# Kernel optimization log

Hardware: AMD Instinct MI355X
Metric: run time of the kernel (lower is better)

## Reference

```python
import jax, jax.numpy as jnp
import numpy as np

N = 6000      # nodes
E = 150000    # edges (avg degree ~25, close to _AVG_DEGREE=23.4)
K = 9         # (lmax+1)^2 spherical coefficients, lmax=2
C = 128       # sphere_channels
H = 8         # num_heads
V = 16        # attn_value_channels (H*V == C)
L = 2         # num_layers
B = 512       # num_distance_basis
RMAX = 5.0
EPS = 1e-6


def _rms_sh(x):
    # rms_norm_sh-style normalization over (coefficients, channels)
    return x * jax.lax.rsqrt(jnp.mean(x * x, axis=(-2, -1), keepdims=True) + EPS)


def _seg_softmax(logits, seg, n):
    # numerically-stable per-destination-node softmax over incoming edges
    m = jax.ops.segment_max(logits, seg, num_segments=n)
    ex = jnp.exp(logits - m[seg])
    s = jax.ops.segment_sum(ex, seg, num_segments=n)
    return ex / (s[seg] + 1e-9)


def setup_inputs() -> dict:
    key = jax.random.key(0)
    ks = jax.random.split(key, 24)
    s = 0.02
    inp = {
        # graph / features
        "atom_feats": jax.random.randint(ks[0], (N, 4), 0, 10),
        "bond_feats": jax.random.randint(ks[1], (E, 3), 0, 8),
        "edge_index": jax.random.randint(ks[2], (2, E), 0, N),
        "edge_distance": jax.random.uniform(ks[3], (E,), jnp.float32, 0.0, RMAX),
        # embeddings
        "atom_emb": jax.random.normal(ks[4], (4, 10, C), jnp.float32) * s,
        "bond_emb": jax.random.normal(ks[5], (3, 8, C), jnp.float32) * s,
        # distance-basis edge MLP (edge_channels_list = [512, 128, 128])
        "W_rbf1": jax.random.normal(ks[6], (B, C), jnp.float32) * s,
        "b_rbf1": jnp.zeros((C,), jnp.float32),
        "W_rbf2": jax.random.normal(ks[7], (C, C), jnp.float32) * s,
        "b_rbf2": jnp.zeros((C,), jnp.float32),
        # per-layer attention params (stacked over L)
        "Wa1": jax.random.normal(ks[8], (L, 3 * C, C), jnp.float32) * s,
        "Wa2": jax.random.normal(ks[9], (L, C, H), jnp.float32) * s,
        "Wv": jax.random.normal(ks[10], (L, C, H * V), jnp.float32) * s,
        "Wg": jax.random.normal(ks[11], (L, C, H), jnp.float32) * s,
        "Wo": jax.random.normal(ks[12], (L, H * V, C), jnp.float32) * s,
        # per-layer FFN params
        "Wf1": jax.random.normal(ks[13], (L, C, 512), jnp.float32) * s,
        "Wf2": jax.random.normal(ks[14], (L, 512, C), jnp.float32) * s,
    }
    return inp


def _forward(atom_feats, bond_feats, edge_index, edge_distance,
             atom_emb, bond_emb, W_rbf1, b_rbf1, W_rbf2, b_rbf2,
             Wa1, Wa2, Wv, Wg, Wo, Wf1, Wf2):
    src, dst = edge_index[0], edge_index[1]

    # --- atom embedding into l=0 coefficient of the SH node state ---
    a0 = sum(atom_emb[f][atom_feats[:, f]] for f in range(4))      # [N, C]
    x = jnp.zeros((N, K, C), a0.dtype).at[:, 0, :].set(a0)          # [N, K, C]

    # --- gaussian distance basis + edge embedding MLP + bond features ---
    centers = jnp.linspace(0.0, RMAX, B)
    width = RMAX / B
    rbf = jnp.exp(-((edge_distance[:, None] - centers[None, :]) / width) ** 2)  # [E, B]
    e = jax.nn.silu(rbf @ W_rbf1 + b_rbf1) @ W_rbf2 + b_rbf2                    # [E, C]
    e = e + sum(bond_emb[f][bond_feats[:, f]] for f in range(3))

    for l in range(L):
        # ---- SO(2)-style graph attention block ----
        xn = _rms_sh(x)
        xs = xn[src]                                                 # [E, K, C] gather
        inv = jnp.concatenate([xn[src, 0], xn[dst, 0], e], axis=-1)  # invariant feats [E, 3C]
        logits = jax.nn.silu(inv @ Wa1[l]) @ Wa2[l]                  # [E, H]
        alpha = _seg_softmax(logits, dst, N)                         # renormalized attention
        gate = jax.nn.sigmoid(e @ Wg[l])                             # edge-embedding gate [E, H]
        v = jnp.einsum('ekc,chv->ekhv', xs, Wv[l].reshape(C, H, V))  # [E, K, H, V]
        v = v * (alpha * gate)[:, None, :, None]
        msg = v.reshape(E, K, H * V)
        agg = jax.ops.segment_sum(msg, dst, num_segments=N)          # scatter [N, K, H*V]
        x = x + jnp.einsum('nkd,dc->nkc', agg, Wo[l])

        # ---- equivariant FFN with separable S2-style activation ----
        xn = _rms_sh(x)
        h = jnp.einsum('nkc,cf->nkf', xn, Wf1[l])                    # [N, K, 512]
        h0 = jax.nn.silu(h[:, :1, :])                                # l=0 scalar path
        hr = h[:, 1:, :] * jax.nn.sigmoid(h[:, :1, :])               # gated l>0 path
        h = jnp.concatenate([h0, hr], axis=1)
        x = x + jnp.einsum('nkf,fc->nkc', h, Wf2[l])

    return _rms_sh(x)


def reference(atom_feats, bond_feats, edge_index, edge_distance,
              atom_emb, bond_emb, W_rbf1, b_rbf1, W_rbf2, b_rbf2,
              Wa1, Wa2, Wv, Wg, Wo, Wf1, Wf2):
    return _forward(atom_feats, bond_feats, edge_index, edge_distance,
                    atom_emb, bond_emb, W_rbf1, b_rbf1, W_rbf2, b_rbf2,
                    Wa1, Wa2, Wv, Wg, Wo, Wf1, Wf2)
```

## Files before the change

kernel.cpp:

```cpp
#include <hip/hip_runtime.h>

#define NN 6000
#define NE 150000
#define TBM 2048
#define TROWS (TBM + 1)

typedef unsigned int uint;
typedef unsigned short ushort;
typedef __attribute__((ext_vector_type(8))) short short8v;
typedef __attribute__((ext_vector_type(4))) float float4v;

__device__ __forceinline__ float siluf(float x) { return x / (1.f + __expf(-x)); }
__device__ __forceinline__ float sigmf(float x) { return 1.f / (1.f + __expf(-x)); }
__device__ __forceinline__ uint pack2bf(float lo, float hi) {
    uint ul = __float_as_uint(lo);
    ul = (ul + 0x7fffu + ((ul >> 16) & 1u)) >> 16;
    uint uh = __float_as_uint(hi);
    uh = ((uh + 0x7fffu + ((uh >> 16) & 1u)) >> 16) << 16;
    return ul | uh;
}
__device__ __forceinline__ ushort f2bf(float f) {
    uint u = __float_as_uint(f);
    return (ushort)((u + 0x7fffu + ((u >> 16) & 1u)) >> 16);
}
__device__ __forceinline__ float2 up2(uint u) {
    return make_float2(__uint_as_float(u << 16), __uint_as_float(u & 0xffff0000u));
}

__global__ __launch_bounds__(256)
void k_prep(const float* __restrict__ W2, const float* __restrict__ b2,
            const float* __restrict__ Wa1, const float* __restrict__ Wg,
            const float* __restrict__ bemb,
            const float* __restrict__ Wf1, const float* __restrict__ Wf2,
            const float* __restrict__ Wv, const float* __restrict__ Wa2,
            const float* __restrict__ Wo,
            float* __restrict__ W2A, float* __restrict__ W2G,
            float* __restrict__ bA, float* __restrict__ bG,
            uint* __restrict__ BAcb, float* __restrict__ BGc,
            ushort* __restrict__ Wf1x, ushort* __restrict__ Wf2x,
            ushort* __restrict__ Wvx, ushort* __restrict__ Wa1sx,
            ushort* __restrict__ Wa1dx, ushort* __restrict__ Wa2x,
            ushort* __restrict__ Wox, int* __restrict__ deg)
{
    __shared__ float w2_s[8][132];
    const int l = blockIdx.y, bx = blockIdx.x, tid = threadIdx.x;
    const float* Wa1e = Wa1 + (size_t)l * 384 * 128 + 256 * 128;
    const float* Wgl  = Wg  + (size_t)l * 128 * 8;

    if (bx < 16) {
        const int i0 = bx * 8;
        for (int q = tid; q < 8 * 32; q += 256) {
            int ni = q >> 5, j4 = (q & 31) * 4;
            *reinterpret_cast<float4*>(&w2_s[ni][j4]) =
                *reinterpret_cast<const float4*>(&W2[(size_t)(i0 + ni) * 128 + j4]);
        }
        __syncthreads();
        const int j = tid & 127, ng = tid >> 7;
        float a[4] = {0.f, 0.f, 0.f, 0.f};
        #pragma unroll 4
        for (int k4 = 0; k4 < 128; k4 += 4) {
            float w0 = Wa1e[(k4 + 0) * 128 + j];
            float w1 = Wa1e[(k4 + 1) * 128 + j];
            float w2v = Wa1e[(k4 + 2) * 128 + j];
            float w3 = Wa1e[(k4 + 3) * 128 + j];
            #pragma unroll
            for (int r = 0; r < 4; ++r) {
                const float4 xv = *reinterpret_cast<const float4*>(&w2_s[ng * 4 + r][k4]);
                a[r] += xv.x * w0 + xv.y * w1 + xv.z * w2v + xv.w * w3;
            }
        }
        #pragma unroll
        for (int r = 0; r < 4; ++r)
            W2A[(size_t)l * 16384 + (size_t)(i0 + ng * 4 + r) * 128 + j] = a[r];
    } else if (bx == 16) {
        const int i = tid & 127, hq = tid >> 7;
        float a[4] = {0.f, 0.f, 0.f, 0.f};
        for (int k = 0; k < 128; ++k) {
            float w = W2[(size_t)i * 128 + k];
            const float4 g4 = *reinterpret_cast<const float4*>(&Wgl[k * 8 + hq * 4]);
            a[0] += w * g4.x; a[1] += w * g4.y; a[2] += w * g4.z; a[3] += w * g4.w;
        }
        #pragma unroll
        for (int q = 0; q < 4; ++q)
            W2G[(size_t)l * 1024 + (size_t)i * 8 + hq * 4 + q] = a[q];
    } else if (bx == 17) {
        if (tid < 128) {
            float s = 0.f;
            for (int k = 0; k < 128; ++k) s += b2[k] * Wa1e[k * 128 + tid];
            bA[l * 128 + tid] = s;
        } else if (tid < 136) {
            int h = tid - 128;
            float s = 0.f;
            for (int k = 0; k < 128; ++k) s += b2[k] * Wgl[k * 8 + h];
            bG[l * 8 + h] = s;
        } else if (l == 0) {
            for (int i = tid - 136; i < NN; i += 120) if (i >= 0) deg[i] = 0;
        }
    } else if (bx < 274) {
        const int cb = (bx - 18) * 2 + (tid >> 7);
        const int c = tid & 127;
        const int b[3] = {cb >> 6, (cb >> 3) & 7, cb & 7};
        float s = 0.f;
        #pragma unroll
        for (int f = 0; f < 3; ++f) {
            const float* er = &bemb[(size_t)(f * 8 + b[f]) * 128];
            for (int k = 0; k < 128; ++k)
                s += er[k] * Wa1e[k * 128 + c];
        }
        float hi = __shfl_down(s, 1, 64);
        if ((c & 1) == 0)
            BAcb[(size_t)l * 512 * 64 + (size_t)cb * 64 + (c >> 1)] = pack2bf(s, hi);
        if (c < 8) {
            float g = 0.f;
            #pragma unroll
            for (int f = 0; f < 3; ++f) {
                const float* er = &bemb[(size_t)(f * 8 + b[f]) * 128];
                for (int k = 0; k < 128; ++k)
                    g += er[k] * Wgl[k * 8 + c];
            }
            BGc[(size_t)l * 512 * 8 + (size_t)cb * 8 + c] = g;
        }
    } else {
        const int sub = (bx - 274) * 4 + (tid >> 6);
        const int lane = tid & 63;
        if (sub < 128) {
            const int nt = sub >> 2, kt = sub & 3;
            const float* src = Wf1 + (size_t)l * 65536;
            ushort* dst = Wf1x + (size_t)l * 65536 + ((size_t)sub * 64 + lane) * 8;
            #pragma unroll
            for (int j = 0; j < 8; ++j)
                dst[j] = f2bf(src[(size_t)(kt * 32 + (lane >> 4) * 8 + j) * 512 + nt * 16 + (lane & 15)]);
        } else if (sub < 256) {
            const int b2x = sub - 128;
            const int nt = b2x >> 4, kt = b2x & 15;
            const float* src = Wf2 + (size_t)l * 65536;
            ushort* dst = Wf2x + (size_t)l * 65536 + ((size_t)b2x * 64 + lane) * 8;
            #pragma unroll
            for (int j = 0; j < 8; ++j)
                dst[j] = f2bf(src[(size_t)(kt * 32 + (lane >> 4) * 8 + j) * 128 + nt * 16 + (lane & 15)]);
        } else if (sub < 352) {
            const int b3 = sub - 256;
            const int mat = b3 >> 5, blk = b3 & 31;
            const int nt = blk >> 2, kt = blk & 3;
            const float* src;
            ushort* dst;
            if (mat == 0)      { src = Wv  + (size_t)l * 16384;             dst = Wvx   + (size_t)l * 16384; }
            else if (mat == 1) { src = Wa1 + (size_t)l * 384 * 128;         dst = Wa1sx + (size_t)l * 16384; }
            else               { src = Wa1 + (size_t)l * 384 * 128 + 16384; dst = Wa1dx + (size_t)l * 16384; }
            dst += ((size_t)blk * 64 + lane) * 8;
            #pragma unroll
            for (int j = 0; j < 8; ++j)
                dst[j] = f2bf(src[(size_t)(kt * 32 + (lane >> 4) * 8 + j) * 128 + nt * 16 + (lane & 15)]);
        } else if (sub < 356) {
            const int kt = sub - 352;
            const int col = lane & 15;
            const float* src = Wa2 + (size_t)l * 128 * 8;
            ushort* dst = Wa2x + (size_t)l * 2048 + ((size_t)kt * 64 + lane) * 8;
            #pragma unroll
            for (int j = 0; j < 8; ++j) {
                int krow = kt * 32 + (lane >> 4) * 8 + j;
                dst[j] = (col < 8) ? f2bf(src[(size_t)krow * 8 + col]) : (ushort)0;
            }
        } else {
            const int blk = sub - 356;
            const int nt = blk >> 2, kt = blk & 3;
            const float* src = Wo + (size_t)l * 16384;
            ushort* dst = Wox + (size_t)l * 16384 + ((size_t)blk * 64 + lane) * 8;
            #pragma unroll
            for (int j = 0; j < 8; ++j)
                dst[j] = f2bf(src[(size_t)(kt * 32 + (lane >> 4) * 8 + j) * 128 + nt * 16 + (lane & 15)]);
        }
    }
}

__device__ __forceinline__
void node_gemm3(const ushort a_s[16][136], int tid, int n0,
                const ushort* __restrict__ Wvx, const ushort* __restrict__ Wa1sx,
                const ushort* __restrict__ Wa1dx,
                uint* __restrict__ Vb, uint* __restrict__ Psb, uint* __restrict__ Pdb)
{
    const int l = tid & 63, wq = tid >> 6;
    const int lr = l & 15, lk = l >> 4;
    #pragma unroll
    for (int jb = 0; jb < 6; ++jb) {
        int job = wq * 6 + jb;
        int mat = job >> 3, nt = job & 7;
        const ushort* W = (mat == 0) ? Wvx : (mat == 1 ? Wa1sx : Wa1dx);
        uint* O = (mat == 0) ? Vb : (mat == 1 ? Psb : Pdb);
        float4v acc = (float4v){0.f, 0.f, 0.f, 0.f};
        #pragma unroll
        for (int ks = 0; ks < 4; ++ks) {
            short8v af = *reinterpret_cast<const short8v*>(&a_s[lr][lk * 8 + ks * 32]);
            short8v bf = *reinterpret_cast<const short8v*>(&W[((size_t)(nt * 4 + ks) * 64 + l) * 8]);
            acc = __builtin_amdgcn_mfma_f32_16x16x32_bf16(af, bf, acc, 0, 0, 0);
        }
        #pragma unroll
        for (int r = 0; r < 4; ++r) {
            float v = acc[r];
            float vn = __shfl_xor(v, 1, 64);
            if ((l & 1) == 0) {
                int row = lk * 4 + r, col = nt * 16 + lr;
                O[(size_t)(n0 + row) * 64 + (col >> 1)] = pack2bf(v, vn);
            }
        }
    }
}

__device__ __forceinline__
void node_gemm3_8w(const ushort a_s[16][136], int tid, int n0,
                   const ushort* __restrict__ Wvx, const ushort* __restrict__ Wa1sx,
                   const ushort* __restrict__ Wa1dx,
                   uint* __restrict__ Vb, uint* __restrict__ Psb, uint* __restrict__ Pdb)
{
    const int l = tid & 63, w = tid >> 6;
    const int lr = l & 15, lk = l >> 4;
    #pragma unroll
    for (int jb = 0; jb < 3; ++jb) {
        int job = w * 3 + jb;
        int mat = job >> 3, nt = job & 7;
        const ushort* W = (mat == 0) ? Wvx : (mat == 1 ? Wa1sx : Wa1dx);
        uint* O = (mat == 0) ? Vb : (mat == 1 ? Psb : Pdb);
        float4v acc = (float4v){0.f, 0.f, 0.f, 0.f};
        #pragma unroll
        for (int ks = 0; ks < 4; ++ks) {
            short8v af = *reinterpret_cast<const short8v*>(&a_s[lr][lk * 8 + ks * 32]);
            short8v bf = *reinterpret_cast<const short8v*>(&W[((size_t)(nt * 4 + ks) * 64 + l) * 8]);
            acc = __builtin_amdgcn_mfma_f32_16x16x32_bf16(af, bf, acc, 0, 0, 0);
        }
        #pragma unroll
        for (int r = 0; r < 4; ++r) {
            float v = acc[r];
            float vn = __shfl_xor(v, 1, 64);
            if ((l & 1) == 0) {
                int row = lk * 4 + r, col = nt * 16 + lr;
                O[(size_t)(n0 + row) * 64 + (col >> 1)] = pack2bf(v, vn);
            }
        }
    }
}

__global__ __launch_bounds__(256)
void k_prep2(const float* __restrict__ W1, const float* __restrict__ b1,
             const float* __restrict__ W2A, const float* __restrict__ W2G,
             const float* __restrict__ bA, const float* __restrict__ bG,
             uint* __restrict__ TAb, float* __restrict__ TG,
             const int* __restrict__ af, const float* __restrict__ aemb,
             float* __restrict__ x, int* __restrict__ deg,
             const int* __restrict__ eidx,
             const ushort* __restrict__ Wvx, const ushort* __restrict__ Wa1sx,
             const ushort* __restrict__ Wa1dx,
             uint* __restrict__ Vb, uint* __restrict__ Psb, uint* __restrict__ Pdb)
{
    __shared__ float rbf_s[8][32];
    __shared__ int   bs_s[8];
    __shared__ float t1_s[8][132];
    __shared__ ushort a_s[16][136];
    const int tid = threadIdx.x, bx = blockIdx.x;

    if (bx < 514) {
        const int l = (bx >= 257) ? 1 : 0;
        const int r0 = (bx - l * 257) * 8;
        {
            int ri = tid >> 5, j = tid & 31;
            int row = min(r0 + ri, TBM);
            float d = (float)row * (5.0f / TBM);
            const float step = 5.0f / 511.0f;
            const float invw = 512.0f / 5.0f;
            int b0 = (int)(d * (511.0f / 5.0f) + 0.5f);
            int bs = min(max(b0 - 16, 0), 512 - 32);
            if (j == 0) bs_s[ri] = bs;
            float z = (d - (float)(bs + j) * step) * invw;
            rbf_s[ri][j] = __expf(-z * z);
        }
        __syncthreads();
        #pragma unroll
        for (int pass = 0; pass < 4; ++pass) {
            int idx = pass * 256 + tid;
            int ri = idx >> 7, c = idx & 127;
            int bs = bs_s[ri];
            float t = b1[c];
            #pragma unroll
            for (int j = 0; j < 32; ++j)
                t += rbf_s[ri][j] * W1[(bs + j) * 128 + c];
            t1_s[ri][c] = siluf(t);
        }
        __syncthreads();

        const float* W2Al = W2A + (size_t)l * 16384;
        const int c = tid & 127, ng = tid >> 7;
        float a[4];
        #pragma unroll
        for (int r = 0; r < 4; ++r) a[r] = bA[l * 128 + c];
        #pragma unroll 4
        for (int k4 = 0; k4 < 128; k4 += 4) {
            float w0 = W2Al[(k4 + 0) * 128 + c];
            float w1 = W2Al[(k4 + 1) * 128 + c];
            float w2v = W2Al[(k4 + 2) * 128 + c];
            float w3 = W2Al[(k4 + 3) * 128 + c];
            #pragma unroll
            for (int r = 0; r < 4; ++r) {
                const float4 xv = *reinterpret_cast<const float4*>(&t1_s[ng * 4 + r][k4]);
                a[r] += xv.x * w0 + xv.y * w1 + xv.z * w2v + xv.w * w3;
            }
        }
        #pragma unroll
        for (int r = 0; r < 4; ++r) {
            float hi = __shfl_down(a[r], 1, 64);
            int row = r0 + ng * 4 + r;
            if (((c & 1) == 0) && row <= TBM)
                TAb[(size_t)l * TROWS * 64 + (size_t)row * 64 + (c >> 1)] = pack2bf(a[r], hi);
        }
        if (tid < 64) {
            int ri = tid >> 3, h = tid & 7;
            int row = r0 + ri;
            if (row <= TBM) {
                const float* W2Gl = W2G + (size_t)l * 1024;
                float s = bG[l * 8 + h];
                #pragma unroll 8
                for (int k = 0; k < 128; ++k)
                    s += t1_s[ri][k] * W2Gl[k * 8 + h];
                TG[(size_t)l * TROWS * 8 + (size_t)row * 8 + h] = s;
            }
        }
    } else if (bx < 889) {
        const int n0 = (bx - 514) * 16;
        {
            int ni = tid >> 4, c8 = (tid & 15) * 8;
            int n = n0 + ni;
            float v[8];
            #pragma unroll
            for (int q = 0; q < 8; ++q) v[q] = 0.f;
            #pragma unroll
            for (int f = 0; f < 4; ++f) {
                int idx = af[n * 4 + f];
                const float* er = &aemb[(size_t)(f * 10 + idx) * 128 + c8];
                float4 e0 = *reinterpret_cast<const float4*>(er);
                float4 e1 = *reinterpret_cast<const float4*>(er + 4);
                v[0] += e0.x; v[1] += e0.y; v[2] += e0.z; v[3] += e0.w;
                v[4] += e1.x; v[5] += e1.y; v[6] += e1.z; v[7] += e1.w;
            }
            float* xr = &x[(size_t)n * 128 + c8];
            *reinterpret_cast<float4*>(xr)     = make_float4(v[0], v[1], v[2], v[3]);
            *reinterpret_cast<float4*>(xr + 4) = make_float4(v[4], v[5], v[6], v[7]);
            float ss = 0.f;
            #pragma unroll
            for (int q = 0; q < 8; ++q) ss += v[q] * v[q];
            #pragma unroll
            for (int m = 1; m < 16; m <<= 1) ss += __shfl_xor(ss, m, 16);
            float r = rsqrtf(ss * (1.0f / 1152.0f) + 1e-6f);
            uint4 pk;
            pk.x = pack2bf(v[0] * r, v[1] * r);
            pk.y = pack2bf(v[2] * r, v[3] * r);
            pk.z = pack2bf(v[4] * r, v[5] * r);
            pk.w = pack2bf(v[6] * r, v[7] * r);
            *reinterpret_cast<uint4*>(&a_s[ni][c8]) = pk;
        }
        __syncthreads();
        node_gemm3(a_s, tid, n0, Wvx, Wa1sx, Wa1dx, Vb, Psb, Pdb);
    } else {
        int e = (bx - 889) * 256 + tid;
        if (e < NE) atomicAdd(&deg[eidx[NE + e]], 1);
    }
}

__global__ __launch_bounds__(1024)
void k_scan(const int* __restrict__ deg, int* __restrict__ off, int* __restrict__ cursor)
{
    __shared__ int part[1024];
    const int t = threadIdx.x;
    const int base = t * 6;
    int loc[6]; int s = 0;
    #pragma unroll
    for (int i = 0; i < 6; ++i) {
        int d = (base + i < NN) ? deg[base + i] : 0;
        loc[i] = s; s += d;
    }
    part[t] = s;
    __syncthreads();
    for (int o = 1; o < 1024; o <<= 1) {
        int v = (t >= o) ? part[t - o] : 0;
        __syncthreads();
        part[t] += v;
        __syncthreads();
    }
    int pre = (t > 0) ? part[t - 1] : 0;
    #pragma unroll
    for (int i = 0; i < 6; ++i) {
        if (base + i < NN) {
            int v = pre + loc[i];
            off[base + i] = v;
            cursor[base + i] = v;
        }
    }
    if (t == 1023) off[NN] = part[1023];
}

__global__ __launch_bounds__(256)
void k_fill(const int* __restrict__ eidx, const int* __restrict__ bondf,
            const float* __restrict__ dist, int* __restrict__ cursor,
            int* __restrict__ srcp, int4* __restrict__ erec)
{
    int e = blockIdx.x * 256 + threadIdx.x;
    if (e < NE) {
        int d = eidx[NE + e];
        int p = atomicAdd(&cursor[d], 1);
        int sn = eidx[e];
        srcp[p] = sn;
        erec[p] = make_int4(sn, d, __float_as_int(dist[e]),
                            bondf[e * 3 + 0] * 64 + bondf[e * 3 + 1] * 8 + bondf[e * 3 + 2]);
    }
}

__global__ __launch_bounds__(256)
void k_attn(const int4* __restrict__ erec,
            const uint* __restrict__ Psb, const uint* __restrict__ Pdb,
            const uint* __restrict__ TAbl, const float* __restrict__ TGl,
            const uint* __restrict__ BAcbl, const float* __restrict__ BGcl,
            const ushort* __restrict__ Wa2xl,
            uint* __restrict__ nexp)
{
    __shared__ ushort t_s[64][136];
    __shared__ float gate_s[64][8];
    const int tid = threadIdx.x;
    const int p0 = blockIdx.x * 64;

    #pragma unroll
    for (int half = 0; half < 2; ++half) {
        const int ei = (tid >> 3) + half * 32;
        const int g = tid & 7;
        const int p = min(p0 + ei, NE - 1);
        const int4 er = erec[p];
        const int sn = er.x, dn = er.y;
        const float d = __int_as_float(er.z);
        const int cb = er.w;
        float u = d * ((float)TBM / 5.0f);
        int i = min((int)u, TBM - 1);
        float f = u - (float)i, f1 = 1.f - f;

        uint ps[8], pd[8], t0[8], t1v[8], ba[8];
        {
            const uint4* pp = reinterpret_cast<const uint4*>(&Psb[(size_t)sn * 64 + g * 8]);
            uint4 a = pp[0], b = pp[1];
            ps[0]=a.x; ps[1]=a.y; ps[2]=a.z; ps[3]=a.w; ps[4]=b.x; ps[5]=b.y; ps[6]=b.z; ps[7]=b.w;
            pp = reinterpret_cast<const uint4*>(&Pdb[(size_t)dn * 64 + g * 8]);
            a = pp[0]; b = pp[1];
            pd[0]=a.x; pd[1]=a.y; pd[2]=a.z; pd[3]=a.w; pd[4]=b.x; pd[5]=b.y; pd[6]=b.z; pd[7]=b.w;
            pp = reinterpret_cast<const uint4*>(&TAbl[(size_t)i * 64 + g * 8]);
            a = pp[0]; b = pp[1];
            t0[0]=a.x; t0[1]=a.y; t0[2]=a.z; t0[3]=a.w; t0[4]=b.x; t0[5]=b.y; t0[6]=b.z; t0[7]=b.w;
            pp = reinterpret_cast<const uint4*>(&TAbl[(size_t)(i + 1) * 64 + g * 8]);
            a = pp[0]; b = pp[1];
            t1v[0]=a.x; t1v[1]=a.y; t1v[2]=a.z; t1v[3]=a.w; t1v[4]=b.x; t1v[5]=b.y; t1v[6]=b.z; t1v[7]=b.w;
            pp = reinterpret_cast<const uint4*>(&BAcbl[(size_t)cb * 64 + g * 8]);
            a = pp[0]; b = pp[1];
            ba[0]=a.x; ba[1]=a.y; ba[2]=a.z; ba[3]=a.w; ba[4]=b.x; ba[5]=b.y; ba[6]=b.z; ba[7]=b.w;
        }
        uint tw[8];
        #pragma unroll
        for (int q = 0; q < 8; ++q) {
            float2 vs = up2(ps[q]), vd = up2(pd[q]), v0 = up2(t0[q]), v1 = up2(t1v[q]), vb = up2(ba[q]);
            float s0 = siluf(vs.x + vd.x + f1 * v0.x + f * v1.x + vb.x);
            float s1 = siluf(vs.y + vd.y + f1 * v0.y + f * v1.y + vb.y);
            tw[q] = pack2bf(s0, s1);
        }
        uint4* tp = reinterpret_cast<uint4*>(&t_s[ei][g * 16]);
        tp[0] = make_uint4(tw[0], tw[1], tw[2], tw[3]);
        tp[1] = make_uint4(tw[4], tw[5], tw[6], tw[7]);
        if (g == 0) {
            const float4* tg0 = reinterpret_cast<const float4*>(&TGl[(size_t)i * 8]);
            const float4* bg4 = reinterpret_cast<const float4*>(&BGcl[(size_t)cb * 8]);
            #pragma unroll
            for (int q = 0; q < 2; ++q) {
                float4 g0 = tg0[q], g1 = tg0[q + 2], bb = bg4[q];
                gate_s[ei][4 * q + 0] = f1 * g0.x + f * g1.x + bb.x;
                gate_s[ei][4 * q + 1] = f1 * g0.y + f * g1.y + bb.y;
                gate_s[ei][4 * q + 2] = f1 * g0.z + f * g1.z + bb.z;
                gate_s[ei][4 * q + 3] = f1 * g0.w + f * g1.w + bb.w;
            }
        }
    }
    __syncthreads();

    {
        const int wq = tid >> 6, l = tid & 63;
        const int lr = l & 15, lk = l >> 4;
        float4v acc = (float4v){0.f, 0.f, 0.f, 0.f};
        #pragma unroll
        for (int ks = 0; ks < 4; ++ks) {
            short8v af = *reinterpret_cast<const short8v*>(&t_s[wq * 16 + lr][lk * 8 + ks * 32]);
            short8v bf = *reinterpret_cast<const short8v*>(&Wa2xl[((size_t)ks * 64 + l) * 8]);
            acc = __builtin_amdgcn_mfma_f32_16x16x32_bf16(af, bf, acc, 0, 0, 0);
        }
        const int h = l & 15;
        if (h < 8) {
            #pragma unroll
            for (int r = 0; r < 4; ++r) {
                int ei = wq * 16 + lk * 4 + r;
                int p = p0 + ei;
                if (p < NE) {
                    float ex = __expf(acc[r]);
                    nexp[(size_t)p * 8 + h] = pack2bf(ex * sigmf(gate_s[ei][h]), ex);
                }
            }
        }
    }
}

template<int LAST>
__global__ __launch_bounds__(512)
void k_layer_fused(float* __restrict__ x,
                   const int* __restrict__ off, const int* __restrict__ srcp,
                   const uint* __restrict__ nexp, const uint* __restrict__ Vb,
                   const ushort* __restrict__ Woxl,
                   const ushort* __restrict__ Wf1xl, const ushort* __restrict__ Wf2xl,
                   float* __restrict__ out,
                   const ushort* __restrict__ WvxN, const ushort* __restrict__ Wa1sxN,
                   const ushort* __restrict__ Wa1dxN,
                   uint* __restrict__ VbO, uint* __restrict__ Psb, uint* __restrict__ Pdb)
{
    __shared__ ushort a_s[16][136];
    __shared__ ushort h_s[16][520];
    __shared__ float xf_s[16][132];
    const int tid = threadIdx.x;
    const int n0 = blockIdx.x * 16;
    const int ni = tid >> 5;
    const int ci = tid & 31;
    const int c4 = ci * 4;

    {
        *reinterpret_cast<float4*>(&xf_s[ni][c4]) =
            *reinterpret_cast<const float4*>(&x[(size_t)(n0 + ni) * 128 + c4]);
    }

    {
        const int n = n0 + ni;
        const int h = ci >> 2;
        const int cd2 = ci * 2;
        const int s = off[n], t = off[n + 1];
        float a0 = 0.f, a1 = 0.f, a2 = 0.f, a3 = 0.f, es = 0.f;
        int p = s;
        for (; p + 4 <= t; p += 4) {
            int sn0 = srcp[p + 0], sn1 = srcp[p + 1], sn2 = srcp[p + 2], sn3 = srcp[p + 3];
            float2 ne0 = up2(nexp[(size_t)(p + 0) * 8 + h]);
            float2 ne1 = up2(nexp[(size_t)(p + 1) * 8 + h]);
            float2 ne2 = up2(nexp[(size_t)(p + 2) * 8 + h]);
            float2 ne3 = up2(nexp[(size_t)(p + 3) * 8 + h]);
            uint2 u0 = *reinterpret_cast<const uint2*>(&Vb[(size_t)sn0 * 64 + cd2]);
            uint2 u1 = *reinterpret_cast<const uint2*>(&Vb[(size_t)sn1 * 64 + cd2]);
            uint2 u2 = *reinterpret_cast<const uint2*>(&Vb[(size_t)sn2 * 64 + cd2]);
            uint2 u3 = *reinterpret_cast<const uint2*>(&Vb[(size_t)sn3 * 64 + cd2]);
            es += ne0.y + ne1.y + ne2.y + ne3.y;
            float2 v;
            v = up2(u0.x); a0 += ne0.x * v.x; a1 += ne0.x * v.y;
            v = up2(u0.y); a2 += ne0.x * v.x; a3 += ne0.x * v.y;
            v = up2(u1.x); a0 += ne1.x * v.x; a1 += ne1.x * v.y;
            v = up2(u1.y); a2 += ne1.x * v.x; a3 += ne1.x * v.y;
            v = up2(u2.x); a0 += ne2.x * v.x; a1 += ne2.x * v.y;
            v = up2(u2.y); a2 += ne2.x * v.x; a3 += ne2.x * v.y;
            v = up2(u3.x); a0 += ne3.x * v.x; a1 += ne3.x * v.y;
            v = up2(u3.y); a2 += ne3.x * v.x; a3 += ne3.x * v.y;
        }
        for (; p < t; ++p) {
            int sn = srcp[p];
            float2 ne = up2(nexp[(size_t)p * 8 + h]);
            uint2 u = *reinterpret_cast<const uint2*>(&Vb[(size_t)sn * 64 + cd2]);
            es += ne.y;
            float2 v;
            v = up2(u.x); a0 += ne.x * v.x; a1 += ne.x * v.y;
            v = up2(u.y); a2 += ne.x * v.x; a3 += ne.x * v.y;
        }
        float sinv = 1.f / (es + 1e-9f);
        uint2 pk;
        pk.x = pack2bf(a0 * sinv, a1 * sinv);
        pk.y = pack2bf(a2 * sinv, a3 * sinv);
        *reinterpret_cast<uint2*>(&a_s[ni][c4]) = pk;
    }
    __syncthreads();

    const int l  = tid & 63;
    const int w  = tid >> 6;
    const int lr = l & 15, lk = l >> 4;

    {
        float4v acc = (float4v){0.f, 0.f, 0.f, 0.f};
        #pragma unroll
        for (int ks = 0; ks < 4; ++ks) {
            short8v af = *reinterpret_cast<const short8v*>(&a_s[lr][lk * 8 + ks * 32]);
            short8v bf = *reinterpret_cast<const short8v*>(&Woxl[((size_t)(w * 4 + ks) * 64 + l) * 8]);
            acc = __builtin_amdgcn_mfma_f32_16x16x32_bf16(af, bf, acc, 0, 0, 0);
        }
        #pragma unroll
        for (int r = 0; r < 4; ++r)
            xf_s[lk * 4 + r][w * 16 + lr] += acc[r];
    }
    __syncthreads();

    {
        float4 v = *reinterpret_cast<const float4*>(&xf_s[ni][c4]);
        float ss = v.x * v.x + v.y * v.y + v.z * v.z + v.w * v.w;
        #pragma unroll
        for (int m = 1; m < 32; m <<= 1) ss += __shfl_xor(ss, m, 32);
        float r = rsqrtf(ss * (1.0f / 1152.0f) + 1e-6f);
        uint2 pk;
        pk.x = pack2bf(v.x * r, v.y * r);
        pk.y = pack2bf(v.z * r, v.w * r);
        *reinterpret_cast<uint2*>(&a_s[ni][c4]) = pk;
    }
    __syncthreads();

    {
        float4v acc[4];
        #pragma unroll
        for (int nf = 0; nf < 4; ++nf) acc[nf] = (float4v){0.f, 0.f, 0.f, 0.f};
        #pragma unroll
        for (int ks = 0; ks < 4; ++ks) {
            short8v af = *reinterpret_cast<const short8v*>(&a_s[lr][lk * 8 + ks * 32]);
            #pragma unroll
            for (int nf = 0; nf < 4; ++nf) {
                int nt = w * 4 + nf;
                short8v bf = *reinterpret_cast<const short8v*>(&Wf1xl[((size_t)(nt * 4 + ks) * 64 + l) * 8]);
                acc[nf] = __builtin_amdgcn_mfma_f32_16x16x32_bf16(af, bf, acc[nf], 0, 0, 0);
            }
        }
        #pragma unroll
        for (int nf = 0; nf < 4; ++nf) {
            #pragma unroll
            for (int r = 0; r < 4; ++r) {
                float v = siluf(acc[nf][r]);
                float vn = __shfl_xor(v, 1, 64);
                if ((l & 1) == 0) {
                    int row = lk * 4 + r;
                    int col = (w * 4 + nf) * 16 + lr;
                    *reinterpret_cast<uint*>(&h_s[row][col]) = pack2bf(v, vn);
                }
            }
        }
    }
    __syncthreads();

    {
        float4v acc = (float4v){0.f, 0.f, 0.f, 0.f};
        #pragma unroll 4
        for (int ks = 0; ks < 16; ++ks) {
            short8v af = *reinterpret_cast<const short8v*>(&h_s[lr][lk * 8 + ks * 32]);
            short8v bf = *reinterpret_cast<const short8v*>(&Wf2xl[((size_t)(w * 16 + ks) * 64 + l) * 8]);
            acc = __builtin_amdgcn_mfma_f32_16x16x32_bf16(af, bf, acc, 0, 0, 0);
        }
        #pragma unroll
        for (int r = 0; r < 4; ++r)
            xf_s[lk * 4 + r][w * 16 + lr] += acc[r];
    }
    __syncthreads();

    {
        float4 v = *reinterpret_cast<const float4*>(&xf_s[ni][c4]);
        float ss = v.x * v.x + v.y * v.y + v.z * v.z + v.w * v.w;
        #pragma unroll
        for (int m = 1; m < 32; m <<= 1) ss += __shfl_xor(ss, m, 32);
        float r = rsqrtf(ss * (1.0f / 1152.0f) + 1e-6f);

        if (!LAST) {
            *reinterpret_cast<float4*>(&x[(size_t)(n0 + ni) * 128 + c4]) = v;
            uint2 pk;
            pk.x = pack2bf(v.x * r, v.y * r);
            pk.y = pack2bf(v.z * r, v.w * r);
            *reinterpret_cast<uint2*>(&a_s[ni][c4]) = pk;
            __syncthreads();
            node_gemm3_8w(a_s, tid, n0, WvxN, Wa1sxN, Wa1dxN, VbO, Psb, Pdb);
        } else {
            size_t base = (size_t)(n0 + ni) * 1152 + c4;
            *reinterpret_cast<float4*>(&out[base]) = make_float4(v.x * r, v.y * r, v.z * r, v.w * r);
            const float4 z4 = make_float4(0.f, 0.f, 0.f, 0.f);
            #pragma unroll
            for (int k = 1; k < 9; ++k)
                *reinterpret_cast<float4*>(&out[base + (size_t)k * 128]) = z4;
        }
    }
}

extern "C" void kernel_launch(void* const* d_in, const int* in_sizes, int n_in,
                              void* d_out, int out_size, void* d_ws, size_t ws_size,
                              hipStream_t stream)
{
    const int*   atom_feats = (const int*)d_in[0];
    const int*   bond_feats = (const int*)d_in[1];
    const int*   edge_index = (const int*)d_in[2];
    const float* edge_dist  = (const float*)d_in[3];
    const float* atom_emb   = (const float*)d_in[4];
    const float* bond_emb   = (const float*)d_in[5];
    const float* W_rbf1     = (const float*)d_in[6];
    const float* b_rbf1     = (const float*)d_in[7];
    const float* W_rbf2     = (const float*)d_in[8];
    const float* b_rbf2     = (const float*)d_in[9];
    const float* Wa1        = (const float*)d_in[10];
    const float* Wa2        = (const float*)d_in[11];
    const float* Wv         = (const float*)d_in[12];
    const float* Wg         = (const float*)d_in[13];
    const float* Wo         = (const float*)d_in[14];
    const float* Wf1        = (const float*)d_in[15];
    const float* Wf2        = (const float*)d_in[16];
    float* out = (float*)d_out;

    float* ws   = (float*)d_ws;
    float* x    = ws;
    uint* nexp  = (uint*)(x + NN * 128);
    float* W2A  = (float*)(nexp + (size_t)NE * 8);
    float* W2G  = W2A  + 2 * 16384;
    float* bA   = W2G  + 2 * 1024;
    float* bG   = bA   + 2 * 128;
    float* TG   = bG   + 16;
    float* BGc  = TG   + 2 * (size_t)TROWS * 8;
    uint* Vb    = (uint*)(BGc + 2 * 512 * 8);
    uint* Psb   = Vb  + NN * 64;
    uint* Pdb   = Psb + NN * 64;
    uint* TAb   = Pdb + NN * 64;
    uint* BAcb  = TAb + 2 * (size_t)TROWS * 64;
    ushort* Wf1x  = (ushort*)(BAcb + 2 * 512 * 64);
    ushort* Wf2x  = Wf1x  + 2 * 65536;
    ushort* Wvx   = Wf2x  + 2 * 65536;
    ushort* Wa1sx = Wvx   + 2 * 16384;
    ushort* Wa1dx = Wa1sx + 2 * 16384;
    ushort* Wa2x  = Wa1dx + 2 * 16384;
    ushort* Wox   = Wa2x  + 2 * 2048;
    int* deg    = (int*)(Wox + 2 * 16384);
    int* off    = deg + NN;
    int* cursor = off + NN + 1;
    int* srcp   = cursor + NN;
    int4* erec  = (int4*)(srcp + NE);

    k_prep<<<dim3(371, 2), 256, 0, stream>>>(W_rbf2, b_rbf2, Wa1, Wg, bond_emb,
        Wf1, Wf2, Wv, Wa2, Wo, W2A, W2G, bA, bG, BAcb, BGc,
        Wf1x, Wf2x, Wvx, Wa1sx, Wa1dx, Wa2x, Wox, deg);
    k_prep2<<<889 + (NE + 255) / 256, 256, 0, stream>>>(W_rbf1, b_rbf1, W2A, W2G, bA, bG,
        TAb, TG, atom_feats, atom_emb, x, deg, edge_index,
        Wvx, Wa1sx, Wa1dx, Vb, Psb, Pdb);

    k_scan<<<1, 1024, 0, stream>>>(deg, off, cursor);
    k_fill<<<(NE + 255) / 256, 256, 0, stream>>>(edge_index, bond_feats, edge_dist,
                                                 cursor, srcp, erec);

    for (int l = 0; l < 2; ++l) {
        k_attn<<<(NE + 63) / 64, 256, 0, stream>>>(erec,
            Psb, Pdb,
            TAb + (size_t)l * TROWS * 64, TG + (size_t)l * TROWS * 8,
            BAcb + (size_t)l * 512 * 64, BGc + (size_t)l * 512 * 8,
            Wa2x + (size_t)l * 2048, nexp);
        if (l == 0)
            k_layer_fused<0><<<NN / 16, 512, 0, stream>>>(x, off, srcp, nexp, Vb,
                Wox, Wf1x, Wf2x, out,
                Wvx + 16384, Wa1sx + 16384, Wa1dx + 16384, Vb, Psb, Pdb);
        else
            k_layer_fused<1><<<NN / 16, 512, 0, stream>>>(x, off, srcp, nexp, Vb,
                Wox + 16384, Wf1x + 65536, Wf2x + 65536, out,
                Wvx, Wa1sx, Wa1dx, Vb, Psb, Pdb);
    }
}
```

Baseline: 149.6 us.

## Compute distance-table second GEMM with bf16 MFMA and 16-row blocks

```diff
diff --git a/kernel.cpp b/kernel.cpp
--- a/kernel.cpp
+++ b/kernel.cpp
@@ -34,7 +34,7 @@
             const float* __restrict__ Wf1, const float* __restrict__ Wf2,
             const float* __restrict__ Wv, const float* __restrict__ Wa2,
             const float* __restrict__ Wo,
-            float* __restrict__ W2A, float* __restrict__ W2G,
+            ushort* __restrict__ W2Ax, float* __restrict__ W2G,
             float* __restrict__ bA, float* __restrict__ bG,
             uint* __restrict__ BAcb, float* __restrict__ BGc,
             ushort* __restrict__ Wf1x, ushort* __restrict__ Wf2x,
@@ -69,9 +69,14 @@
                 a[r] += xv.x * w0 + xv.y * w1 + xv.z * w2v + xv.w * w3;
             }
         }
-        #pragma unroll
-        for (int r = 0; r < 4; ++r)
-            W2A[(size_t)l * 16384 + (size_t)(i0 + ng * 4 + r) * 128 + j] = a[r];
+        const int nt = j >> 4;
+        #pragma unroll
+        for (int r = 0; r < 4; ++r) {
+            int row = i0 + ng * 4 + r;
+            int kt = row >> 5, jj = row & 7;
+            int lane = ((row >> 3) & 3) * 16 + (j & 15);
+            W2Ax[(size_t)l * 16384 + ((size_t)(nt * 4 + kt) * 64 + lane) * 8 + jj] = f2bf(a[r]);
+        }
     } else if (bx == 16) {
         const int i = tid & 127, hq = tid >> 7;
         float a[4] = {0.f, 0.f, 0.f, 0.f};
@@ -241,7 +246,7 @@
 
 __global__ __launch_bounds__(256)
 void k_prep2(const float* __restrict__ W1, const float* __restrict__ b1,
-             const float* __restrict__ W2A, const float* __restrict__ W2G,
+             const ushort* __restrict__ W2Ax, const float* __restrict__ W2G,
              const float* __restrict__ bA, const float* __restrict__ bG,
              uint* __restrict__ TAb, float* __restrict__ TG,
              const int* __restrict__ af, const float* __restrict__ aemb,
@@ -251,17 +256,19 @@
              const ushort* __restrict__ Wa1dx,
              uint* __restrict__ Vb, uint* __restrict__ Psb, uint* __restrict__ Pdb)
 {
-    __shared__ float rbf_s[8][32];
-    __shared__ int   bs_s[8];
-    __shared__ float t1_s[8][132];
+    __shared__ float rbf_s[16][32];
+    __shared__ int   bs_s[16];
+    __shared__ float t1_s[16][132];
     __shared__ ushort a_s[16][136];
     const int tid = threadIdx.x, bx = blockIdx.x;
 
-    if (bx < 514) {
-        const int l = (bx >= 257) ? 1 : 0;
-        const int r0 = (bx - l * 257) * 8;
-        {
-            int ri = tid >> 5, j = tid & 31;
+    if (bx < 258) {
+        const int l = (bx >= 129) ? 1 : 0;
+        const int r0 = (bx - l * 129) * 16;
+        #pragma unroll
+        for (int pass = 0; pass < 2; ++pass) {
+            int idx = pass * 256 + tid;
+            int ri = idx >> 5, j = idx & 31;
             int row = min(r0 + ri, TBM);
             float d = (float)row * (5.0f / TBM);
             const float step = 5.0f / 511.0f;
@@ -274,7 +281,7 @@
         }
         __syncthreads();
         #pragma unroll
-        for (int pass = 0; pass < 4; ++pass) {
+        for (int pass = 0; pass < 8; ++pass) {
             int idx = pass * 256 + tid;
             int ri = idx >> 7, c = idx & 127;
             int bs = bs_s[ri];
@@ -282,35 +289,40 @@
             #pragma unroll
             for (int j = 0; j < 32; ++j)
                 t += rbf_s[ri][j] * W1[(bs + j) * 128 + c];
-            t1_s[ri][c] = siluf(t);
+            t = siluf(t);
+            t1_s[ri][c] = t;
+            float hi = __shfl_down(t, 1, 64);
+            if ((c & 1) == 0)
+                *reinterpret_cast<uint*>(&a_s[ri][c]) = pack2bf(t, hi);
         }
         __syncthreads();
 
-        const float* W2Al = W2A + (size_t)l * 16384;
-        const int c = tid & 127, ng = tid >> 7;
-        float a[4];
-        #pragma unroll
-        for (int r = 0; r < 4; ++r) a[r] = bA[l * 128 + c];
-        #pragma unroll 4
-        for (int k4 = 0; k4 < 128; k4 += 4) {
-            float w0 = W2Al[(k4 + 0) * 128 + c];
-            float w1 = W2Al[(k4 + 1) * 128 + c];
-            float w2v = W2Al[(k4 + 2) * 128 + c];
-            float w3 = W2Al[(k4 + 3) * 128 + c];
+        const int l64 = tid & 63, wq = tid >> 6;
+        const int lr = l64 & 15, lk = l64 >> 4;
+        const ushort* W2Axl = W2Ax + (size_t)l * 16384;
+        #pragma unroll
+        for (int nf = 0; nf < 2; ++nf) {
+            int nt = wq * 2 + nf;
+            float bAv = bA[l * 128 + nt * 16 + lr];
+            float4v acc = (float4v){bAv, bAv, bAv, bAv};
+            #pragma unroll
+            for (int ks = 0; ks < 4; ++ks) {
+                short8v afr = *reinterpret_cast<const short8v*>(&a_s[lr][lk * 8 + ks * 32]);
+                short8v bfr = *reinterpret_cast<const short8v*>(&W2Axl[((size_t)(nt * 4 + ks) * 64 + l64) * 8]);
+                acc = __builtin_amdgcn_mfma_f32_16x16x32_bf16(afr, bfr, acc, 0, 0, 0);
+            }
             #pragma unroll
             for (int r = 0; r < 4; ++r) {
-                const float4 xv = *reinterpret_cast<const float4*>(&t1_s[ng * 4 + r][k4]);
-                a[r] += xv.x * w0 + xv.y * w1 + xv.z * w2v + xv.w * w3;
-            }
-        }
-        #pragma unroll
-        for (int r = 0; r < 4; ++r) {
-            float hi = __shfl_down(a[r], 1, 64);
-            int row = r0 + ng * 4 + r;
-            if (((c & 1) == 0) && row <= TBM)
-                TAb[(size_t)l * TROWS * 64 + (size_t)row * 64 + (c >> 1)] = pack2bf(a[r], hi);
-        }
-        if (tid < 64) {
+                float v = acc[r];
+                float vn = __shfl_xor(v, 1, 64);
+                int row = r0 + lk * 4 + r;
+                int col = nt * 16 + lr;
+                if (((l64 & 1) == 0) && row <= TBM)
+                    TAb[(size_t)l * TROWS * 64 + (size_t)row * 64 + (col >> 1)] = pack2bf(v, vn);
+            }
+        }
+
+        if (tid < 128) {
             int ri = tid >> 3, h = tid & 7;
             int row = r0 + ri;
             if (row <= TBM) {
@@ -322,8 +334,8 @@
                 TG[(size_t)l * TROWS * 8 + (size_t)row * 8 + h] = s;
             }
         }
-    } else if (bx < 889) {
-        const int n0 = (bx - 514) * 16;
+    } else if (bx < 633) {
+        const int n0 = (bx - 258) * 16;
         {
             int ni = tid >> 4, c8 = (tid & 15) * 8;
             int n = n0 + ni;
@@ -358,7 +370,7 @@
         __syncthreads();
         node_gemm3(a_s, tid, n0, Wvx, Wa1sx, Wa1dx, Vb, Psb, Pdb);
     } else {
-        int e = (bx - 889) * 256 + tid;
+        int e = (bx - 633) * 256 + tid;
         if (e < NE) atomicAdd(&deg[eidx[NE + e]], 1);
     }
 }
@@ -704,8 +716,7 @@
     float* ws   = (float*)d_ws;
     float* x    = ws;
     uint* nexp  = (uint*)(x + NN * 128);
-    float* W2A  = (float*)(nexp + (size_t)NE * 8);
-    float* W2G  = W2A  + 2 * 16384;
+    float* W2G  = (float*)(nexp + (size_t)NE * 8);
     float* bA   = W2G  + 2 * 1024;
     float* bG   = bA   + 2 * 128;
     float* TG   = bG   + 16;
@@ -722,16 +733,17 @@
     ushort* Wa1dx = Wa1sx + 2 * 16384;
     ushort* Wa2x  = Wa1dx + 2 * 16384;
     ushort* Wox   = Wa2x  + 2 * 2048;
-    int* deg    = (int*)(Wox + 2 * 16384);
+    ushort* W2Ax  = Wox   + 2 * 16384;
+    int* deg    = (int*)(W2Ax + 2 * 16384);
     int* off    = deg + NN;
     int* cursor = off + NN + 1;
     int* srcp   = cursor + NN;
     int4* erec  = (int4*)(srcp + NE);
 
     k_prep<<<dim3(371, 2), 256, 0, stream>>>(W_rbf2, b_rbf2, Wa1, Wg, bond_emb,
-        Wf1, Wf2, Wv, Wa2, Wo, W2A, W2G, bA, bG, BAcb, BGc,
+        Wf1, Wf2, Wv, Wa2, Wo, W2Ax, W2G, bA, bG, BAcb, BGc,
         Wf1x, Wf2x, Wvx, Wa1sx, Wa1dx, Wa2x, Wox, deg);
-    k_prep2<<<889 + (NE + 255) / 256, 256, 0, stream>>>(W_rbf1, b_rbf1, W2A, W2G, bA, bG,
+    k_prep2<<<633 + (NE + 255) / 256, 256, 0, stream>>>(W_rbf1, b_rbf1, W2Ax, W2G, bA, bG,
         TAb, TG, atom_feats, atom_emb, x, deg, edge_index,
         Wvx, Wa1sx, Wa1dx, Vb, Psb, Pdb);
 
```

Result: no change. 151.9 us (+1.5%).
